# Kernel optimization log

Measured on AMD Instinct MI355X. Metric: run time of the kernel, lower is better.

## Reference

```python
import jax, jax.numpy as jnp
import numpy as np

NEG_SLOPE = 0.2  # GATConv default negative_slope


def gat_conv(x, row, col, W, b, a_src, a_dst, N):
    # GATConv, heads=1, flow='target_to_source': i=row (central), j=col (neighbor)
    h = x @ W                                                   # [N, C]
    e = jax.nn.leaky_relu((h @ a_src)[col] + (h @ a_dst)[row], NEG_SLOPE)  # [E]
    m = jax.ops.segment_max(e, row, num_segments=N)             # segment softmax over row
    w = jnp.exp(e - m[row])
    denom = jax.ops.segment_sum(w, row, num_segments=N)
    alpha = w / (denom[row] + 1e-16)
    out = jax.ops.segment_sum(alpha[:, None] * h[col], row, num_segments=N)
    return out + b


def lstm_scan(xs_t, Wih, Whh, bih, bhh):
    # xs_t: [L, N, C] -> hidden states [L, N, H]; PyTorch gate order i,f,g,o
    H = Whh.shape[1]
    Nn = xs_t.shape[1]
    bias = bih + bhh
    def step(carry, xt):
        h, c = carry
        g = xt @ Wih.T + h @ Whh.T + bias
        i, f, gg, o = jnp.split(g, 4, axis=-1)
        c = jax.nn.sigmoid(f) * c + jax.nn.sigmoid(i) * jnp.tanh(gg)
        h = jax.nn.sigmoid(o) * jnp.tanh(c)
        return (h, c), h
    init = (jnp.zeros((Nn, H), xs_t.dtype), jnp.zeros((Nn, H), xs_t.dtype))
    _, hs = jax.lax.scan(step, init, xs_t)
    return hs


def jk_lstm(xst, Wih_f, Whh_f, bih_f, bhh_f, Wih_b, Whh_b, bih_b, bhh_b, att_W, att_b):
    # xst: [L, N, C]; bidirectional LSTM over layer dim, attention-weighted sum
    hf = lstm_scan(xst, Wih_f, Whh_f, bih_f, bhh_f)
    hb = lstm_scan(xst[::-1], Wih_b, Whh_b, bih_b, bhh_b)[::-1]
    h = jnp.concatenate([hf, hb], axis=-1)                      # [L, N, 2H]
    score = jnp.einsum('lnh,h->ln', h, att_W) + att_b           # [L, N]
    alpha = jax.nn.softmax(score, axis=0)                       # softmax over layers
    return jnp.einsum('lnc,ln->nc', xst, alpha)                 # [N, C]


def setup_inputs() -> dict:
    key = jax.random.key(0)
    ks = list(jax.random.split(key, 32))
    N, E, C = 50000, 800000, 128
    L = 3
    H = (L * C) // 2  # 192; PyG JumpingKnowledge lstm hidden size
    s = 0.05
    d = {}
    d['x'] = jax.random.normal(ks[0], (N, 3), jnp.float32)
    d['edge_index'] = jax.random.randint(ks[1], (2, E), 0, N, jnp.int64)
    d['gat_W0'] = jax.random.normal(ks[2], (3, C)) * 0.3
    d['gat_b0'] = jnp.zeros((C,))
    d['gat_as0'] = jax.random.normal(ks[3], (C,)) * s
    d['gat_ad0'] = jax.random.normal(ks[4], (C,)) * s
    d['gat_W'] = jax.random.normal(ks[5], (L - 1, C, C)) * s
    d['gat_b'] = jnp.zeros((L - 1, C))
    d['gat_as'] = jax.random.normal(ks[6], (L - 1, C)) * s
    d['gat_ad'] = jax.random.normal(ks[7], (L - 1, C)) * s
    d['lstm_Wih_f'] = jax.random.normal(ks[8], (4 * H, C)) * s
    d['lstm_Whh_f'] = jax.random.normal(ks[9], (4 * H, H)) * s
    d['lstm_bih_f'] = jnp.zeros((4 * H,))
    d['lstm_bhh_f'] = jnp.zeros((4 * H,))
    d['lstm_Wih_b'] = jax.random.normal(ks[10], (4 * H, C)) * s
    d['lstm_Whh_b'] = jax.random.normal(ks[11], (4 * H, H)) * s
    d['lstm_bih_b'] = jnp.zeros((4 * H,))
    d['lstm_bhh_b'] = jnp.zeros((4 * H,))
    d['att_W'] = jax.random.normal(ks[12], (2 * H,)) * s
    d['att_b'] = jnp.zeros((1,))
    d['nW1'] = jax.random.normal(ks[13], (C, C)) * s
    d['nb1'] = jnp.zeros((C,))
    d['nW2'] = jax.random.normal(ks[14], (C, 2)) * s
    d['nb2'] = jnp.zeros((2,))
    d['eW1'] = jax.random.normal(ks[15], (2 * C, C)) * s
    d['eb1'] = jnp.zeros((C,))
    d['eW2'] = jax.random.normal(ks[16], (C, 2)) * s
    d['eb2'] = jnp.zeros((2,))
    return d


def reference(x, edge_index, gat_W0, gat_b0, gat_as0, gat_ad0, gat_W, gat_b, gat_as, gat_ad,
              lstm_Wih_f, lstm_Whh_f, lstm_bih_f, lstm_bhh_f,
              lstm_Wih_b, lstm_Whh_b, lstm_bih_b, lstm_bhh_b,
              att_W, att_b, nW1, nb1, nW2, nb2, eW1, eb1, eW2, eb2):
    N = x.shape[0]
    row, col = edge_index[0], edge_index[1]
    xs = []
    h = jax.nn.relu(gat_conv(x, row, col, gat_W0, gat_b0, gat_as0, gat_ad0, N))
    xs.append(h)
    for l in range(gat_W.shape[0]):  # fixed small layer count
        h = jax.nn.relu(gat_conv(h, row, col, gat_W[l], gat_b[l], gat_as[l], gat_ad[l], N))
        xs.append(h)
    xst = jnp.stack(xs, axis=0)  # [L, N, C]
    h = jk_lstm(xst, lstm_Wih_f, lstm_Whh_f, lstm_bih_f, lstm_bhh_f,
                lstm_Wih_b, lstm_Whh_b, lstm_bih_b, lstm_bhh_b, att_W, att_b)
    # node classifier (dropout is identity in eval)
    node_out = jax.nn.softmax(jax.nn.relu(h @ nW1 + nb1) @ nW2 + nb2, axis=1)
    # edge representation gather + concat, then edge classifier
    edge_rep = jnp.concatenate([h[row], h[col]], axis=1)  # [E, 2C]
    edge_out = jax.nn.softmax(jax.nn.relu(edge_rep @ eW1 + eb1) @ eW2 + eb2, axis=1)
    return node_out, edge_out
```

## Files before the change

kernel.cpp:

```cpp
#include <hip/hip_runtime.h>
#include <cstdint>
#include <cstddef>


#define NIN 28
#define MAXJOBS 20

struct InPtrs { const void* p[NIN]; int n[NIN]; };

struct ConvJobs {
    const void* src[MAXJOBS];
    float* dst[MAXJOBS];
    int n[MAXJOBS];
    int ai[MAXJOBS];
    int blk0[MAXJOBS + 1];
    int njobs;
};

typedef short s16x4 __attribute__((ext_vector_type(4)));
typedef short s16x8 __attribute__((ext_vector_type(8)));
typedef float f32x4 __attribute__((ext_vector_type(4)));
typedef unsigned short u16x8 __attribute__((ext_vector_type(8)));

__device__ __forceinline__ float bf2f(unsigned short v) {
    unsigned int u = ((unsigned int)v) << 16;
    return __uint_as_float(u);
}

__device__ __forceinline__ unsigned short f2bf(float x) {
    unsigned int u = __float_as_uint(x);
    unsigned int r = u + 0x7fffu + ((u >> 16) & 1u);
    return (unsigned short)(r >> 16);
}

__device__ __forceinline__ float rdx(const void* p, size_t i, int isf32) {
    return isf32 ? ((const float*)p)[i] : bf2f(((const unsigned short*)p)[i]);
}

__device__ __forceinline__ float frcp(float x) {
    return __builtin_amdgcn_rcpf(x);
}

__device__ __forceinline__ float sigm(float x) {
    return frcp(1.f + __expf(-x));
}

__device__ __forceinline__ float fast_tanh(float x) {
    return 1.f - 2.f * frcp(__expf(2.f * x) + 1.f);
}

__global__ void k_sniff(InPtrs in, int* flags) {
    int ai = blockIdx.x;
    if (ai >= NIN) return;
    __shared__ int cnt;
    if (threadIdx.x == 0) cnt = 0;
    __syncthreads();
    if (ai == 1) {
        const int* w = (const int*)in.p[1];
        int nw = in.n[1] < 512 ? in.n[1] : 512;
        int local = 0;
        for (int i = threadIdx.x; i < nw; i += blockDim.x)
            if ((i & 1) && w[i] != 0) local++;
        atomicAdd(&cnt, local);
        __syncthreads();
        if (threadIdx.x == 0) flags[1] = (cnt < 4) ? 1 : 0;
        return;
    }
    const unsigned short* u = (const unsigned short*)in.p[ai];
    int ns = in.n[ai] < 256 ? in.n[ai] : 256;
    int local = 0;
    for (int i = threadIdx.x; i < ns; i += blockDim.x) {
        if (i & 1) continue;
        unsigned short v = u[i];
        int e = (v >> 7) & 0xff;
        if ((v & 0x7fff) != 0 && (e < 100 || e > 154)) local++;
    }
    atomicAdd(&cnt, local);
    __syncthreads();
    if (threadIdx.x == 0) flags[ai] = (cnt * 4 >= ns) ? 1 : 0;
}

__global__ void k_convall(ConvJobs J, const int* __restrict__ flags) {
    int b = blockIdx.x;
    int j = 0;
    while (j + 1 < J.njobs && b >= J.blk0[j + 1]) ++j;
    int i = (b - J.blk0[j]) * 256 + threadIdx.x;
    if (i >= J.n[j]) return;
    J.dst[j][i] = rdx(J.src[j], i, flags[J.ai[j]]);
}

__global__ void k_conve(const void* src, int* row, int* col, int* cnt,
                        int E, const int* flags) {
    int i = blockIdx.x * blockDim.x + threadIdx.x;
    if (i >= E) return;
    int r, c;
    if (flags[1]) {
        const long long* s = (const long long*)src;
        r = (int)s[i];
        c = (int)s[(size_t)E + i];
    } else {
        const int* s = (const int*)src;
        r = s[i];
        c = s[(size_t)E + i];
    }
    row[i] = r;
    col[i] = c;
    atomicAdd(&cnt[r], 1);
}

__global__ void k_scan1(const int* __restrict__ deg, int* __restrict__ indptr,
                        int* __restrict__ bsums, int N) {
    __shared__ int buf[1024];
    const int t = threadIdx.x;
    const int base = blockIdx.x * 1024;
    int v = (base + t < N) ? deg[base + t] : 0;
    buf[t] = v;
    __syncthreads();
    for (int ofs = 1; ofs < 1024; ofs <<= 1) {
        int add = (t >= ofs) ? buf[t - ofs] : 0;
        __syncthreads();
        buf[t] += add;
        __syncthreads();
    }
    if (base + t < N) indptr[base + t] = buf[t] - v;
    if (t == 1023) bsums[blockIdx.x] = buf[1023];
}

__global__ void k_scan2(int* bsums, int nb) {
    if (threadIdx.x == 0 && blockIdx.x == 0) {
        int acc = 0;
        for (int j = 0; j < nb; ++j) { int v = bsums[j]; bsums[j] = acc; acc += v; }
        bsums[nb] = acc;
    }
}

__global__ void k_scan3(const int* __restrict__ bsums, int* __restrict__ indptr,
                        int* __restrict__ cnt, int N, int nb) {
    int i = blockIdx.x * blockDim.x + threadIdx.x;
    if (i < N) {
        indptr[i] += bsums[i >> 10];
        cnt[i] = 0;
    }
    if (i == 0) indptr[N] = bsums[nb];
}

__global__ void k_fill(const int* __restrict__ row, const int* __restrict__ col,
                       const int* __restrict__ indptr, int* __restrict__ cur,
                       int* __restrict__ colS, int* __restrict__ eidx, int E) {
    int i = blockIdx.x * blockDim.x + threadIdx.x;
    if (i >= E) return;
    int r = row[i];
    int p = indptr[r] + atomicAdd(&cur[r], 1);
    colS[p] = col[i];
    eidx[p] = i;
}

__global__ __launch_bounds__(256) void k_lin0(
    const float* __restrict__ x, const float* __restrict__ W0,
    const float* __restrict__ asrc, const float* __restrict__ adst,
    unsigned short* __restrict__ hlin, float* __restrict__ hs, float* __restrict__ hd,
    int N) {
    const int wid = threadIdx.x >> 6, lane = threadIdx.x & 63;
    const int n = blockIdx.x * 4 + wid;
    if (n >= N) return;
    float x0 = x[(size_t)n * 3], x1 = x[(size_t)n * 3 + 1], x2 = x[(size_t)n * 3 + 2];
    const int c0 = lane, c1 = lane + 64;
    float h0 = x0 * W0[c0] + x1 * W0[128 + c0] + x2 * W0[256 + c0];
    float h1 = x0 * W0[c1] + x1 * W0[128 + c1] + x2 * W0[256 + c1];
    hlin[(size_t)n * 128 + c0] = f2bf(h0);
    hlin[(size_t)n * 128 + c1] = f2bf(h1);
    float sp = h0 * asrc[c0] + h1 * asrc[c1];
    float dp = h0 * adst[c0] + h1 * adst[c1];
    for (int o = 32; o; o >>= 1) { sp += __shfl_down(sp, o); dp += __shfl_down(dp, o); }
    if (lane == 0) { hs[n] = sp; hd[n] = dp; }
}

__global__ void k_wpackg(const float* __restrict__ Wcanon,
                         unsigned short* __restrict__ Wg) {
    int idx = blockIdx.x * blockDim.x + threadIdx.x;
    if (idx >= 2 * 4 * 8 * 512) return;
    int layer = idx / 16384;
    int r  = idx % 16384;
    int kb = r / 4096;
    int r2 = r % 4096;
    int f  = r2 / 512;
    int q  = r2 % 512;
    int lane = q >> 3, j = q & 7;
    int k   = kb * 32 + ((j >> 2) * 16) + ((lane >> 4) * 4) + (j & 3);
    int col = f * 16 + (lane & 15);
    Wg[idx] = f2bf(Wcanon[(size_t)layer * 16384 + (size_t)k * 128 + col]);
}

__global__ __launch_bounds__(512) void k_linm(
    const unsigned short* __restrict__ xin,
    const unsigned short* __restrict__ Wg,
    const float* __restrict__ asrc, const float* __restrict__ adst,
    unsigned short* __restrict__ hlin, float* __restrict__ hs, float* __restrict__ hd,
    int N) {
    __shared__ unsigned short AS[64][136];
    __shared__ float hsS[64], hdS[64];
    const int t = threadIdx.x;
    const int f = t >> 6, lane = t & 63;
    const int n0 = blockIdx.x * 64;
    const int ccol = lane & 15;
    const int klane = lane >> 4;
    const int lrow = klane * 4;
    const int akl = klane * 4;
    const int m = f * 16 + ccol;

    const float asv = asrc[m], adv = adst[m];

    for (int i = t; i < 1024; i += 512) {
        int r = i >> 4, kq = (i & 15) * 8;
        u16x8 v = (u16x8)(0);
        if (n0 + r < N) v = *(const u16x8*)(xin + (size_t)(n0 + r) * 128 + kq);
        *(u16x8*)&AS[r][kq] = v;
    }
    if (t < 64) { hsS[t] = 0.f; hdS[t] = 0.f; }
    __syncthreads();

    f32x4 acc[4];
    #pragma unroll
    for (int rf = 0; rf < 4; ++rf) acc[rf] = (f32x4)(0.f);
    #pragma unroll
    for (int kb = 0; kb < 4; ++kb) {
        s16x8 b = *(const s16x8*)(Wg + ((size_t)kb * 8 + f) * 512 + lane * 8);
        const int k0 = kb * 32 + akl;
        #pragma unroll
        for (int rf = 0; rf < 4; ++rf) {
            s16x4 alo = *(const s16x4*)&AS[rf * 16 + ccol][k0];
            s16x4 ahi = *(const s16x4*)&AS[rf * 16 + ccol][k0 + 16];
            s16x8 av = __builtin_shufflevector(alo, ahi, 0, 1, 2, 3, 4, 5, 6, 7);
            acc[rf] = __builtin_amdgcn_mfma_f32_16x16x32_bf16(av, b, acc[rf], 0, 0, 0);
        }
    }
    __syncthreads();

    float sp[16], dp[16];
    #pragma unroll
    for (int rf = 0; rf < 4; ++rf) {
        #pragma unroll
        for (int reg = 0; reg < 4; ++reg) {
            float h = acc[rf][reg];
            int ci = rf * 4 + reg;
            AS[rf * 16 + lrow + reg][m] = f2bf(h);
            sp[ci] = h * asv;
            dp[ci] = h * adv;
        }
    }
    #pragma unroll
    for (int o = 1; o < 16; o <<= 1) {
        #pragma unroll
        for (int i = 0; i < 16; ++i) { sp[i] += __shfl_xor(sp[i], o); dp[i] += __shfl_xor(dp[i], o); }
    }
    if (ccol == 0) {
        #pragma unroll
        for (int i = 0; i < 16; ++i) {
            int row = (i >> 2) * 16 + lrow + (i & 3);
            atomicAdd(&hsS[row], sp[i]);
            atomicAdd(&hdS[row], dp[i]);
        }
    }
    __syncthreads();

    for (int i = t; i < 1024; i += 512) {
        int r = i >> 4, kq = (i & 15) * 8;
        if (n0 + r < N)
            *(u16x8*)(hlin + (size_t)(n0 + r) * 128 + kq) = *(const u16x8*)&AS[r][kq];
    }
    if (t < 64 && n0 + t < N) { hs[n0 + t] = hsS[t]; hd[n0 + t] = hdS[t]; }
}

__global__ __launch_bounds__(256) void k_aggr(
    const unsigned short* __restrict__ hlin, const float* __restrict__ hs,
    const float* __restrict__ hd,
    const int* __restrict__ indptr, const int* __restrict__ colS,
    const float* __restrict__ b, unsigned short* __restrict__ xout, int N) {
    const int wid = threadIdx.x >> 6, lane = threadIdx.x & 63;
    const int n = blockIdx.x * 4 + wid;
    if (n >= N) return;
    const int s = indptr[n], epos = indptr[n + 1];
    const float hdv = hd[n];
    const int c0 = lane, c1 = lane + 64;
    float m = -1e30f, d = 0.f, a0 = 0.f, a1 = 0.f;
    int idx = s;
    for (; idx + 8 <= epos; idx += 8) {
        int cl[8];
        #pragma unroll
        for (int j = 0; j < 8; ++j) cl[j] = colS[idx + j];
        float e[8];
        #pragma unroll
        for (int j = 0; j < 8; ++j) {
            float ev = hs[cl[j]] + hdv;
            e[j] = (ev > 0.f) ? ev : 0.2f * ev;
        }
        float v0[8], v1[8];
        #pragma unroll
        for (int j = 0; j < 8; ++j) {
            const unsigned short* hp = hlin + (size_t)cl[j] * 128;
            v0[j] = bf2f(hp[c0]);
            v1[j] = bf2f(hp[c1]);
        }
        float m8 = e[0];
        #pragma unroll
        for (int j = 1; j < 8; ++j) m8 = fmaxf(m8, e[j]);
        if (m8 > m) {
            float sc = __expf(m - m8);
            a0 *= sc; a1 *= sc; d *= sc; m = m8;
        }
        #pragma unroll
        for (int j = 0; j < 8; ++j) {
            float w = __expf(e[j] - m);
            a0 += w * v0[j];
            a1 += w * v1[j];
            d  += w;
        }
    }
    for (; idx < epos; ++idx) {
        int col = colS[idx];
        float e = hs[col] + hdv;
        e = (e > 0.f) ? e : 0.2f * e;
        const unsigned short* hr = hlin + (size_t)col * 128;
        float v0 = bf2f(hr[c0]), v1 = bf2f(hr[c1]);
        if (e > m) {
            float sc = __expf(m - e);
            a0 = a0 * sc + v0;
            a1 = a1 * sc + v1;
            d  = d * sc + 1.f;
            m  = e;
        } else {
            float w = __expf(e - m);
            a0 += w * v0;
            a1 += w * v1;
            d  += w;
        }
    }
    float inv = frcp(d + 1e-16f);
    float r0 = a0 * inv + b[c0];
    float r1 = a1 * inv + b[c1];
    xout[(size_t)n * 128 + c0] = f2bf(fmaxf(r0, 0.f));
    xout[(size_t)n * 128 + c1] = f2bf(fmaxf(r1, 0.f));
}

__global__ void k_wpack(const void* Wihf, const void* Whhf,
                        const void* Wihb, const void* Whhb,
                        const void* bihf, const void* bhhf,
                        const void* bihb, const void* bhhb,
                        const int* __restrict__ flags,
                        unsigned short* __restrict__ Bpack, float* __restrict__ bsum) {
    int idx = blockIdx.x * blockDim.x + threadIdx.x;
    const int TOT = 2 * 10 * 48 * 512;
    if (idx < TOT) {
        int dir = idx / (10 * 48 * 512);
        int r   = idx % (10 * 48 * 512);
        int kb  = r / (48 * 512);
        int r2  = r % (48 * 512);
        int f   = r2 / 512;
        int q   = r2 % 512;
        int lane = q >> 3, j = q & 7;
        int k   = kb * 32 + ((j >> 2) * 16) + ((lane >> 4) * 4) + (j & 3);
        int col = f * 16 + (lane & 15);
        float v;
        if (k < 128)
            v = dir ? rdx(Wihb, (size_t)col * 128 + k, flags[14])
                    : rdx(Wihf, (size_t)col * 128 + k, flags[10]);
        else
            v = dir ? rdx(Whhb, (size_t)col * 192 + (k - 128), flags[15])
                    : rdx(Whhf, (size_t)col * 192 + (k - 128), flags[11]);
        Bpack[idx] = f2bf(v);
    }
    if (idx < 2 * 768) {
        int d = idx / 768, j = idx % 768;
        bsum[idx] = d ? rdx(bihb, j, flags[16]) + rdx(bhhb, j, flags[17])
                      : rdx(bihf, j, flags[12]) + rdx(bhhf, j, flags[13]);
    }
}

__global__ __launch_bounds__(768, 3) void k_lstm_mfma(
    const unsigned short* __restrict__ xsb,
    const unsigned short* __restrict__ Bpack,
    const float* __restrict__ bsum,
    const float* __restrict__ attW,
    float* __restrict__ scoreP,
    int N) {
    __shared__ unsigned short AS[64][332];
    __shared__ float scoreS[64];
    const int t = threadIdx.x;
    const int bf = t >> 6, lane = t & 63;
    const int dir = blockIdx.y;
    const int n0 = blockIdx.x * 64;
    const int ccol = lane & 15;
    const int klane = lane >> 4;
    const int lrow = klane * 4;
    const int akl = klane * 4;
    const int m = bf * 16 + ccol;

    const float bI = bsum[dir * 768 + m];
    const float bF = bsum[dir * 768 + 192 + m];
    const float bG = bsum[dir * 768 + 384 + m];
    const float bO = bsum[dir * 768 + 576 + m];
    const float awt = attW[dir * 192 + m];
    float cst[16];
    #pragma unroll
    for (int i = 0; i < 16; ++i) cst[i] = 0.f;

    const unsigned short* Bd = Bpack + (size_t)dir * 10 * 48 * 512;

    for (int s = 0; s < 3; ++s) {
        const int l = dir ? (2 - s) : s;
        {
            const unsigned short* xsrc = xsb + ((size_t)l * N + n0) * 128;
            for (int i = t; i < 1024; i += 768) {
                int r = i >> 4, kq = (i & 15) * 8;
                u16x8 v = (u16x8)(0);
                if (n0 + r < N) v = *(const u16x8*)(xsrc + (size_t)r * 128 + kq);
                *(u16x8*)&AS[r][kq] = v;
            }
        }
        if (t < 64) scoreS[t] = 0.f;
        __syncthreads();

        const int KB = s ? 10 : 4;
        f32x4 acc[4][4];
        #pragma unroll
        for (int rf = 0; rf < 4; ++rf)
            #pragma unroll
            for (int g = 0; g < 4; ++g) acc[rf][g] = (f32x4)(0.f);
        s16x8 bA[4], bB[4];
        {
            const unsigned short* bb = Bd + (size_t)bf * 512 + lane * 8;
            #pragma unroll
            for (int g = 0; g < 4; ++g) bA[g] = *(const s16x8*)(bb + (size_t)g * 6144);
        }
        for (int kb = 0; kb < KB; kb += 2) {
            {
                const unsigned short* bb = Bd + ((size_t)(kb + 1) * 48 + bf) * 512 + lane * 8;
                #pragma unroll
                for (int g = 0; g < 4; ++g) bB[g] = *(const s16x8*)(bb + (size_t)g * 6144);
            }
            {
                const int k0 = kb * 32 + akl;
                s16x8 av[4];
                #pragma unroll
                for (int rf = 0; rf < 4; ++rf) {
                    s16x4 alo = *(const s16x4*)&AS[rf * 16 + ccol][k0];
                    s16x4 ahi = *(const s16x4*)&AS[rf * 16 + ccol][k0 + 16];
                    av[rf] = __builtin_shufflevector(alo, ahi, 0, 1, 2, 3, 4, 5, 6, 7);
                }
                #pragma unroll
                for (int rf = 0; rf < 4; ++rf)
                    #pragma unroll
                    for (int g = 0; g < 4; ++g)
                        acc[rf][g] = __builtin_amdgcn_mfma_f32_16x16x32_bf16(
                            av[rf], bA[g], acc[rf][g], 0, 0, 0);
            }
            if (kb + 2 < KB) {
                const unsigned short* bb = Bd + ((size_t)(kb + 2) * 48 + bf) * 512 + lane * 8;
                #pragma unroll
                for (int g = 0; g < 4; ++g) bA[g] = *(const s16x8*)(bb + (size_t)g * 6144);
            }
            {
                const int k0 = (kb + 1) * 32 + akl;
                s16x8 av[4];
                #pragma unroll
                for (int rf = 0; rf < 4; ++rf) {
                    s16x4 alo = *(const s16x4*)&AS[rf * 16 + ccol][k0];
                    s16x4 ahi = *(const s16x4*)&AS[rf * 16 + ccol][k0 + 16];
                    av[rf] = __builtin_shufflevector(alo, ahi, 0, 1, 2, 3, 4, 5, 6, 7);
                }
                #pragma unroll
                for (int rf = 0; rf < 4; ++rf)
                    #pragma unroll
                    for (int g = 0; g < 4; ++g)
                        acc[rf][g] = __builtin_amdgcn_mfma_f32_16x16x32_bf16(
                            av[rf], bB[g], acc[rf][g], 0, 0, 0);
            }
        }
        __syncthreads();

        float sp[16];
        #pragma unroll
        for (int rf = 0; rf < 4; ++rf) {
            #pragma unroll
            for (int reg = 0; reg < 4; ++reg) {
                float gI = acc[rf][0][reg] + bI;
                float gF = acc[rf][1][reg] + bF;
                float gG = acc[rf][2][reg] + bG;
                float gO = acc[rf][3][reg] + bO;
                float ig = sigm(gI);
                float fg = sigm(gF);
                float gt = fast_tanh(gG);
                float og = sigm(gO);
                int ci = rf * 4 + reg;
                float cn = fg * cst[ci] + ig * gt;
                cst[ci] = cn;
                float hh = og * fast_tanh(cn);
                AS[rf * 16 + lrow + reg][128 + m] = f2bf(hh);
                sp[ci] = hh * awt;
            }
        }
        #pragma unroll
        for (int o = 1; o < 16; o <<= 1) {
            #pragma unroll
            for (int i = 0; i < 16; ++i) sp[i] += __shfl_xor(sp[i], o);
        }
        if (ccol == 0) {
            #pragma unroll
            for (int i = 0; i < 16; ++i)
                atomicAdd(&scoreS[(i >> 2) * 16 + lrow + (i & 3)], sp[i]);
        }
        __syncthreads();
        if (t < 64 && n0 + t < N)
            scoreP[(size_t)(dir * 3 + l) * N + n0 + t] = scoreS[t];
    }
}

__global__ __launch_bounds__(256) void k_tail(
    const unsigned short* __restrict__ xsb, const float* __restrict__ scoreP,
    const float* __restrict__ nW1, const float* __restrict__ nb1,
    const float* __restrict__ nW2, const float* __restrict__ nb2,
    const float* __restrict__ eW1, const float* __restrict__ eb1,
    unsigned short* __restrict__ P, unsigned short* __restrict__ Q,
    float* __restrict__ out, int N) {
    __shared__ float xl[16][128];
    __shared__ float al[16][4];
    const int t = threadIdx.x;
    const int wid = t >> 6, lane = t & 63;
    const int nb = blockIdx.x * 16;
    if (t < 16) {
        int n = nb + t;
        float e0 = 0.f, e1 = 0.f, e2 = 0.f;
        if (n < N) {
            float s0 = scoreP[n]                 + scoreP[(size_t)3 * N + n];
            float s1 = scoreP[(size_t)N + n]     + scoreP[(size_t)4 * N + n];
            float s2 = scoreP[(size_t)2 * N + n] + scoreP[(size_t)5 * N + n];
            float mm = fmaxf(s0, fmaxf(s1, s2));
            e0 = __expf(s0 - mm); e1 = __expf(s1 - mm); e2 = __expf(s2 - mm);
            float inv = frcp(e0 + e1 + e2);
            e0 *= inv; e1 *= inv; e2 *= inv;
        }
        al[t][0] = e0; al[t][1] = e1; al[t][2] = e2;
    }
    __syncthreads();
    const size_t L1o = (size_t)N * 128, L2o = 2 * L1o;
    for (int i = t; i < 2048; i += 256) {
        int r = i >> 7, k = i & 127;
        int n = nb + r;
        float v = 0.f;
        if (n < N) {
            size_t p = (size_t)n * 128 + k;
            v = al[r][0] * bf2f(xsb[p]) + al[r][1] * bf2f(xsb[L1o + p])
              + al[r][2] * bf2f(xsb[L2o + p]);
        }
        xl[r][k] = v;
    }
    __syncthreads();
    const int c0 = lane, c1 = lane + 64;
    const int r0 = wid * 4;
    {
        float h0[4], h1[4];
        #pragma unroll
        for (int j = 0; j < 4; ++j) { h0[j] = 0.f; h1[j] = 0.f; }
        #pragma unroll 2
        for (int k = 0; k < 128; ++k) {
            float w0 = nW1[k * 128 + c0], w1 = nW1[k * 128 + c1];
            #pragma unroll
            for (int j = 0; j < 4; ++j) {
                float xv = xl[r0 + j][k];
                h0[j] += xv * w0;
                h1[j] += xv * w1;
            }
        }
        float p0[4], p1[4];
        #pragma unroll
        for (int j = 0; j < 4; ++j) {
            float a = fmaxf(h0[j] + nb1[c0], 0.f);
            float bq = fmaxf(h1[j] + nb1[c1], 0.f);
            p0[j] = a * nW2[c0 * 2 + 0] + bq * nW2[c1 * 2 + 0];
            p1[j] = a * nW2[c0 * 2 + 1] + bq * nW2[c1 * 2 + 1];
        }
        #pragma unroll
        for (int o = 32; o; o >>= 1) {
            #pragma unroll
            for (int j = 0; j < 4; ++j) {
                p0[j] += __shfl_down(p0[j], o);
                p1[j] += __shfl_down(p1[j], o);
            }
        }
        if (lane == 0) {
            #pragma unroll
            for (int j = 0; j < 4; ++j) {
                int n = nb + r0 + j;
                if (n < N) {
                    float l0 = p0[j] + nb2[0], l1 = p1[j] + nb2[1];
                    float mm = fmaxf(l0, l1);
                    float e0 = __expf(l0 - mm), e1 = __expf(l1 - mm);
                    float inv = frcp(e0 + e1);
                    out[2 * (size_t)n]     = e0 * inv;
                    out[2 * (size_t)n + 1] = e1 * inv;
                }
            }
        }
    }
    {
        float pp0[4], pp1[4], qq0[4], qq1[4];
        #pragma unroll
        for (int j = 0; j < 4; ++j) { pp0[j] = 0.f; pp1[j] = 0.f; qq0[j] = 0.f; qq1[j] = 0.f; }
        for (int k = 0; k < 128; ++k) {
            float wp0 = eW1[k * 128 + c0], wp1 = eW1[k * 128 + c1];
            float wq0 = eW1[(128 + k) * 128 + c0], wq1 = eW1[(128 + k) * 128 + c1];
            #pragma unroll
            for (int j = 0; j < 4; ++j) {
                float xv = xl[r0 + j][k];
                pp0[j] += xv * wp0; pp1[j] += xv * wp1;
                qq0[j] += xv * wq0; qq1[j] += xv * wq1;
            }
        }
        #pragma unroll
        for (int j = 0; j < 4; ++j) {
            int n = nb + r0 + j;
            if (n < N) {
                P[(size_t)n * 128 + c0] = f2bf(pp0[j] + eb1[c0]);
                P[(size_t)n * 128 + c1] = f2bf(pp1[j] + eb1[c1]);
                Q[(size_t)n * 128 + c0] = f2bf(qq0[j]);
                Q[(size_t)n * 128 + c1] = f2bf(qq1[j]);
            }
        }
    }
}

__global__ __launch_bounds__(256) void k_edge3(
    const unsigned short* __restrict__ P, const unsigned short* __restrict__ Q,
    const int* __restrict__ indptr, const int* __restrict__ colS,
    const int* __restrict__ eidx,
    const float* __restrict__ W2, const float* __restrict__ b2,
    float* __restrict__ out, int N) {
    const int wid = threadIdx.x >> 6, lane = threadIdx.x & 63;
    const int n = blockIdx.x * 4 + wid;
    if (n >= N) return;
    const int sl = lane & 15, g = lane >> 4;
    const int s = indptr[n], e = indptr[n + 1];
    float pf[8];
    {
        u16x8 pv = *(const u16x8*)(P + (size_t)n * 128 + sl * 8);
        #pragma unroll
        for (int j = 0; j < 8; ++j) pf[j] = bf2f(pv[j]);
    }
    const float* W2f = W2;
    const float b20 = b2[0], b21 = b2[1];
    for (int p = s + g; p < e; p += 8) {
        int p1 = p + 4;
        bool v1 = p1 < e;
        int col0 = colS[p],  eo0 = eidx[p];
        int col1 = v1 ? colS[p1] : col0;
        int eo1  = v1 ? eidx[p1] : 0;
        u16x8 qv0 = *(const u16x8*)(Q + (size_t)col0 * 128 + sl * 8);
        u16x8 qv1 = *(const u16x8*)(Q + (size_t)col1 * 128 + sl * 8);
        float l00 = 0.f, l01 = 0.f, l10 = 0.f, l11 = 0.f;
        #pragma unroll
        for (int j = 0; j < 8; ++j) {
            int ch = sl * 8 + j;
            float wA = W2f[ch * 2], wB = W2f[ch * 2 + 1];
            float h0 = fmaxf(pf[j] + bf2f(qv0[j]), 0.f);
            float h1 = fmaxf(pf[j] + bf2f(qv1[j]), 0.f);
            l00 += h0 * wA; l01 += h0 * wB;
            l10 += h1 * wA; l11 += h1 * wB;
        }
        #pragma unroll
        for (int o = 1; o < 16; o <<= 1) {
            l00 += __shfl_xor(l00, o); l01 += __shfl_xor(l01, o);
            l10 += __shfl_xor(l10, o); l11 += __shfl_xor(l11, o);
        }
        if (sl == 0) {
            {
                float a = l00 + b20, b = l01 + b21;
                float mm = fmaxf(a, b);
                float e0 = __expf(a - mm), e1 = __expf(b - mm);
                float inv = frcp(e0 + e1);
                out[2 * (size_t)N + 2 * (size_t)eo0]     = e0 * inv;
                out[2 * (size_t)N + 2 * (size_t)eo0 + 1] = e1 * inv;
            }
            if (v1) {
                float a = l10 + b20, b = l11 + b21;
                float mm = fmaxf(a, b);
                float e0 = __expf(a - mm), e1 = __expf(b - mm);
                float inv = frcp(e0 + e1);
                out[2 * (size_t)N + 2 * (size_t)eo1]     = e0 * inv;
                out[2 * (size_t)N + 2 * (size_t)eo1 + 1] = e1 * inv;
            }
        }
    }
}

extern "C" void kernel_launch(void* const* d_in, const int* in_sizes, int n_in,
                              void* d_out, int out_size, void* d_ws, size_t ws_size,
                              hipStream_t stream) {
    if (n_in < NIN) return;
    const int N = in_sizes[0] / 3;
    const int E = in_sizes[1] / 2;

    char* ws = (char*)d_ws;
    size_t off = 0;
    auto alloc = [&](size_t bytes) -> char* {
        char* p = ws + off;
        off = (off + bytes + 255) & ~(size_t)255;
        return p;
    };
    int* flags = (int*)alloc(32 * sizeof(int));
    int* bsums = (int*)alloc(128 * sizeof(int));
    float* canon[NIN];
    for (int i = 0; i < NIN; ++i) canon[i] = nullptr;
    for (int i = 0; i < NIN; ++i) {
        if (i == 1 || (i >= 10 && i <= 17)) continue;
        canon[i] = (float*)alloc((size_t)in_sizes[i] * 4);
    }
    int* row32  = (int*)alloc((size_t)E * 4);
    int* col32  = (int*)alloc((size_t)E * 4);
    int* indptr = (int*)alloc((size_t)(N + 1) * 4);
    int* cnt    = (int*)alloc((size_t)N * 4);
    int* colS   = (int*)alloc((size_t)E * 4);
    int* eidx   = (int*)alloc((size_t)E * 4);
    float* hs   = (float*)alloc((size_t)N * 4);
    float* hd   = (float*)alloc((size_t)N * 4);
    float* hJK  = (float*)alloc((size_t)N * 128 * 4);
    unsigned short* hlin = (unsigned short*)hJK;
    unsigned short* xsb = (unsigned short*)alloc((size_t)3 * N * 128 * 2);
    unsigned short* Bpack = (unsigned short*)alloc((size_t)2 * 10 * 48 * 512 * 2);
    unsigned short* Wg = (unsigned short*)alloc((size_t)2 * 4 * 8 * 512 * 2);
    float* bsum = (float*)alloc((size_t)2 * 768 * 4);
    float* scoreP = (float*)alloc((size_t)6 * N * 4);
    if (off > ws_size) return;
    unsigned short* P = (unsigned short*)hJK;
    unsigned short* Q = (unsigned short*)hJK + (size_t)N * 128;

    InPtrs ip;
    for (int i = 0; i < NIN; ++i) { ip.p[i] = d_in[i]; ip.n[i] = in_sizes[i]; }

    k_sniff<<<NIN, 256, 0, stream>>>(ip, flags);

    {
        ConvJobs J;
        int nj = 0, blk = 0;
        for (int i = 0; i < NIN; ++i) {
            if (i == 1 || (i >= 10 && i <= 17)) continue;
            J.src[nj] = d_in[i];
            J.dst[nj] = canon[i];
            J.n[nj] = in_sizes[i];
            J.ai[nj] = i;
            J.blk0[nj] = blk;
            blk += (in_sizes[i] + 255) / 256;
            ++nj;
        }
        J.blk0[nj] = blk;
        J.njobs = nj;
        k_convall<<<blk, 256, 0, stream>>>(J, flags);
    }
    hipMemsetAsync(cnt, 0, (size_t)N * 4, stream);
    k_conve<<<(E + 255) / 256, 256, 0, stream>>>(d_in[1], row32, col32, cnt, E, flags);
    k_wpack<<<(2 * 10 * 48 * 512 + 255) / 256, 256, 0, stream>>>(
        d_in[10], d_in[11], d_in[14], d_in[15],
        d_in[12], d_in[13], d_in[16], d_in[17], flags, Bpack, bsum);
    k_wpackg<<<(2 * 4 * 8 * 512 + 255) / 256, 256, 0, stream>>>(canon[6], Wg);

    const int nb1k = (N + 1023) / 1024;
    k_scan1<<<nb1k, 1024, 0, stream>>>(cnt, indptr, bsums, N);
    k_scan2<<<1, 64, 0, stream>>>(bsums, nb1k);
    k_scan3<<<(N + 255) / 256, 256, 0, stream>>>(bsums, indptr, cnt, N, nb1k);
    k_fill<<<(E + 255) / 256, 256, 0, stream>>>(row32, col32, indptr, cnt, colS, eidx, E);

    k_lin0<<<(N + 3) / 4, 256, 0, stream>>>(canon[0], canon[2], canon[4], canon[5],
                                            hlin, hs, hd, N);
    k_aggr<<<(N + 3) / 4, 256, 0, stream>>>(hlin, hs, hd, indptr, colS, canon[3], xsb, N);
    for (int l = 1; l < 3; ++l) {
        const unsigned short* Wgl = Wg + (size_t)(l - 1) * 4 * 8 * 512;
        const float* bb = canon[7] + (size_t)(l - 1) * 128;
        const float* as = canon[8] + (size_t)(l - 1) * 128;
        const float* ad = canon[9] + (size_t)(l - 1) * 128;
        k_linm<<<(N + 63) / 64, 512, 0, stream>>>(xsb + (size_t)(l - 1) * N * 128, Wgl,
                                                  as, ad, hlin, hs, hd, N);
        k_aggr<<<(N + 3) / 4, 256, 0, stream>>>(hlin, hs, hd, indptr, colS, bb,
                                                xsb + (size_t)l * N * 128, N);
    }

    dim3 lgrid((N + 63) / 64, 2);
    k_lstm_mfma<<<lgrid, 768, 0, stream>>>(xsb, Bpack, bsum, canon[18], scoreP, N);

    float* out = (float*)d_out;
    k_tail<<<(N + 15) / 16, 256, 0, stream>>>(xsb, scoreP,
                                              canon[20], canon[21], canon[22], canon[23],
                                              canon[24], canon[25], P, Q, out, N);
    k_edge3<<<(N + 3) / 4, 256, 0, stream>>>(P, Q, indptr, colS, eidx,
                                             canon[26], canon[27], out, N);
}
```

Measured before the change: 671.7 us.

## Move tail node and edge-projection GEMMs onto bf16 MFMA with packed weights

Replaces the scalar-FMA k_tail kernel with k_tailm, which blends the three layer outputs into a bf16 LDS tile of 64 nodes and computes the node-classifier hidden layer and both edge projections (P and Q) with 16x16x32 bf16 MFMA instructions. A new packing kernel pre-arranges nW1 and both halves of eW1 into the MFMA fragment layout. Outputs are staged through LDS for vectorized coalesced stores, and the node logits are reduced with shuffles and LDS atomics. The aim is to remove the FP32 scalar-FMA cost of three 128x128 GEMMs per node. The trade-off is bf16 rounding of the blended activations and of the weights.

```diff
diff --git a/kernel.cpp b/kernel.cpp
--- a/kernel.cpp
+++ b/kernel.cpp
@@ -189,6 +189,25 @@
     int k   = kb * 32 + ((j >> 2) * 16) + ((lane >> 4) * 4) + (j & 3);
     int col = f * 16 + (lane & 15);
     Wg[idx] = f2bf(Wcanon[(size_t)layer * 16384 + (size_t)k * 128 + col]);
+}
+
+__global__ void k_wpackt(const float* __restrict__ nW1, const float* __restrict__ eW1,
+                         unsigned short* __restrict__ Wt) {
+    int idx = blockIdx.x * blockDim.x + threadIdx.x;
+    if (idx >= 4 * 24 * 512) return;
+    int kb = idx / (24 * 512);
+    int r  = idx % (24 * 512);
+    int fr = r / 512;
+    int q  = r % 512;
+    int lane = q >> 3, j = q & 7;
+    int k   = kb * 32 + ((j >> 2) * 16) + ((lane >> 4) * 4) + (j & 3);
+    int grp = fr >> 3;
+    int col = (fr & 7) * 16 + (lane & 15);
+    float v;
+    if (grp == 0)      v = nW1[(size_t)k * 128 + col];
+    else if (grp == 1) v = eW1[(size_t)k * 128 + col];
+    else               v = eW1[(size_t)(128 + k) * 128 + col];
+    Wt[idx] = f2bf(v);
 }
 
 __global__ __launch_bounds__(512) void k_linm(
@@ -515,20 +534,27 @@
     }
 }
 
-__global__ __launch_bounds__(256) void k_tail(
+__global__ __launch_bounds__(512) void k_tailm(
     const unsigned short* __restrict__ xsb, const float* __restrict__ scoreP,
-    const float* __restrict__ nW1, const float* __restrict__ nb1,
-    const float* __restrict__ nW2, const float* __restrict__ nb2,
-    const float* __restrict__ eW1, const float* __restrict__ eb1,
+    const unsigned short* __restrict__ Wt,
+    const float* __restrict__ nb1, const float* __restrict__ nW2,
+    const float* __restrict__ nb2, const float* __restrict__ eb1,
     unsigned short* __restrict__ P, unsigned short* __restrict__ Q,
     float* __restrict__ out, int N) {
-    __shared__ float xl[16][128];
-    __shared__ float al[16][4];
+    __shared__ unsigned short AS[64][136];
+    __shared__ float al[64][4];
+    __shared__ float lgt[64][2];
     const int t = threadIdx.x;
-    const int wid = t >> 6, lane = t & 63;
-    const int nb = blockIdx.x * 16;
-    if (t < 16) {
-        int n = nb + t;
+    const int f = t >> 6, lane = t & 63;
+    const int n0 = blockIdx.x * 64;
+    const int ccol = lane & 15;
+    const int klane = lane >> 4;
+    const int lrow = klane * 4;
+    const int akl = klane * 4;
+    const int m = f * 16 + ccol;
+
+    if (t < 64) {
+        int n = n0 + t;
         float e0 = 0.f, e1 = 0.f, e2 = 0.f;
         if (n < N) {
             float s0 = scoreP[n]                 + scoreP[(size_t)3 * N + n];
@@ -540,92 +566,110 @@
             e0 *= inv; e1 *= inv; e2 *= inv;
         }
         al[t][0] = e0; al[t][1] = e1; al[t][2] = e2;
-    }
-    __syncthreads();
+        lgt[t][0] = 0.f; lgt[t][1] = 0.f;
+    }
+    __syncthreads();
+
     const size_t L1o = (size_t)N * 128, L2o = 2 * L1o;
-    for (int i = t; i < 2048; i += 256) {
-        int r = i >> 7, k = i & 127;
-        int n = nb + r;
-        float v = 0.f;
-        if (n < N) {
-            size_t p = (size_t)n * 128 + k;
-            v = al[r][0] * bf2f(xsb[p]) + al[r][1] * bf2f(xsb[L1o + p])
-              + al[r][2] * bf2f(xsb[L2o + p]);
-        }
-        xl[r][k] = v;
-    }
-    __syncthreads();
-    const int c0 = lane, c1 = lane + 64;
-    const int r0 = wid * 4;
+    for (int i = t; i < 1024; i += 512) {
+        int r = i >> 4, kq = (i & 15) * 8;
+        u16x8 o8 = (u16x8)(0);
+        if (n0 + r < N) {
+            size_t base = (size_t)(n0 + r) * 128 + kq;
+            u16x8 a = *(const u16x8*)(xsb + base);
+            u16x8 b = *(const u16x8*)(xsb + L1o + base);
+            u16x8 c = *(const u16x8*)(xsb + L2o + base);
+            float w0 = al[r][0], w1 = al[r][1], w2 = al[r][2];
+            #pragma unroll
+            for (int j = 0; j < 8; ++j)
+                o8[j] = f2bf(w0 * bf2f(a[j]) + w1 * bf2f(b[j]) + w2 * bf2f(c[j]));
+        }
+        *(u16x8*)&AS[r][kq] = o8;
+    }
+    __syncthreads();
+
+    f32x4 accN[4], accP[4], accQ[4];
+    #pragma unroll
+    for (int rf = 0; rf < 4; ++rf) { accN[rf] = (f32x4)(0.f); accP[rf] = (f32x4)(0.f); accQ[rf] = (f32x4)(0.f); }
+    #pragma unroll
+    for (int kb = 0; kb < 4; ++kb) {
+        s16x8 bN = *(const s16x8*)(Wt + ((size_t)kb * 24 + f) * 512 + lane * 8);
+        s16x8 bP = *(const s16x8*)(Wt + ((size_t)kb * 24 + 8 + f) * 512 + lane * 8);
+        s16x8 bQ = *(const s16x8*)(Wt + ((size_t)kb * 24 + 16 + f) * 512 + lane * 8);
+        const int k0 = kb * 32 + akl;
+        #pragma unroll
+        for (int rf = 0; rf < 4; ++rf) {
+            s16x4 alo = *(const s16x4*)&AS[rf * 16 + ccol][k0];
+            s16x4 ahi = *(const s16x4*)&AS[rf * 16 + ccol][k0 + 16];
+            s16x8 av = __builtin_shufflevector(alo, ahi, 0, 1, 2, 3, 4, 5, 6, 7);
+            accN[rf] = __builtin_amdgcn_mfma_f32_16x16x32_bf16(av, bN, accN[rf], 0, 0, 0);
+            accP[rf] = __builtin_amdgcn_mfma_f32_16x16x32_bf16(av, bP, accP[rf], 0, 0, 0);
+            accQ[rf] = __builtin_amdgcn_mfma_f32_16x16x32_bf16(av, bQ, accQ[rf], 0, 0, 0);
+        }
+    }
+    __syncthreads();
+
     {
-        float h0[4], h1[4];
-        #pragma unroll
-        for (int j = 0; j < 4; ++j) { h0[j] = 0.f; h1[j] = 0.f; }
-        #pragma unroll 2
-        for (int k = 0; k < 128; ++k) {
-            float w0 = nW1[k * 128 + c0], w1 = nW1[k * 128 + c1];
-            #pragma unroll
-            for (int j = 0; j < 4; ++j) {
-                float xv = xl[r0 + j][k];
-                h0[j] += xv * w0;
-                h1[j] += xv * w1;
-            }
-        }
-        float p0[4], p1[4];
-        #pragma unroll
-        for (int j = 0; j < 4; ++j) {
-            float a = fmaxf(h0[j] + nb1[c0], 0.f);
-            float bq = fmaxf(h1[j] + nb1[c1], 0.f);
-            p0[j] = a * nW2[c0 * 2 + 0] + bq * nW2[c1 * 2 + 0];
-            p1[j] = a * nW2[c0 * 2 + 1] + bq * nW2[c1 * 2 + 1];
-        }
-        #pragma unroll
-        for (int o = 32; o; o >>= 1) {
-            #pragma unroll
-            for (int j = 0; j < 4; ++j) {
-                p0[j] += __shfl_down(p0[j], o);
-                p1[j] += __shfl_down(p1[j], o);
-            }
-        }
-        if (lane == 0) {
-            #pragma unroll
-            for (int j = 0; j < 4; ++j) {
-                int n = nb + r0 + j;
-                if (n < N) {
-                    float l0 = p0[j] + nb2[0], l1 = p1[j] + nb2[1];
-                    float mm = fmaxf(l0, l1);
-                    float e0 = __expf(l0 - mm), e1 = __expf(l1 - mm);
-                    float inv = frcp(e0 + e1);
-                    out[2 * (size_t)n]     = e0 * inv;
-                    out[2 * (size_t)n + 1] = e1 * inv;
-                }
+        const float nb1v = nb1[m];
+        const float w20 = nW2[2 * m], w21 = nW2[2 * m + 1];
+        float s0[16], s1[16];
+        #pragma unroll
+        for (int rf = 0; rf < 4; ++rf) {
+            #pragma unroll
+            for (int reg = 0; reg < 4; ++reg) {
+                float h = fmaxf(accN[rf][reg] + nb1v, 0.f);
+                int ci = rf * 4 + reg;
+                s0[ci] = h * w20;
+                s1[ci] = h * w21;
+            }
+        }
+        #pragma unroll
+        for (int o = 1; o < 16; o <<= 1) {
+            #pragma unroll
+            for (int i = 0; i < 16; ++i) { s0[i] += __shfl_xor(s0[i], o); s1[i] += __shfl_xor(s1[i], o); }
+        }
+        if (ccol == 0) {
+            #pragma unroll
+            for (int i = 0; i < 16; ++i) {
+                int row = (i >> 2) * 16 + lrow + (i & 3);
+                atomicAdd(&lgt[row][0], s0[i]);
+                atomicAdd(&lgt[row][1], s1[i]);
             }
         }
     }
     {
-        float pp0[4], pp1[4], qq0[4], qq1[4];
-        #pragma unroll
-        for (int j = 0; j < 4; ++j) { pp0[j] = 0.f; pp1[j] = 0.f; qq0[j] = 0.f; qq1[j] = 0.f; }
-        for (int k = 0; k < 128; ++k) {
-            float wp0 = eW1[k * 128 + c0], wp1 = eW1[k * 128 + c1];
-            float wq0 = eW1[(128 + k) * 128 + c0], wq1 = eW1[(128 + k) * 128 + c1];
-            #pragma unroll
-            for (int j = 0; j < 4; ++j) {
-                float xv = xl[r0 + j][k];
-                pp0[j] += xv * wp0; pp1[j] += xv * wp1;
-                qq0[j] += xv * wq0; qq1[j] += xv * wq1;
-            }
-        }
-        #pragma unroll
-        for (int j = 0; j < 4; ++j) {
-            int n = nb + r0 + j;
-            if (n < N) {
-                P[(size_t)n * 128 + c0] = f2bf(pp0[j] + eb1[c0]);
-                P[(size_t)n * 128 + c1] = f2bf(pp1[j] + eb1[c1]);
-                Q[(size_t)n * 128 + c0] = f2bf(qq0[j]);
-                Q[(size_t)n * 128 + c1] = f2bf(qq1[j]);
-            }
-        }
+        const float eb1v = eb1[m];
+        #pragma unroll
+        for (int rf = 0; rf < 4; ++rf)
+            #pragma unroll
+            for (int reg = 0; reg < 4; ++reg)
+                AS[rf * 16 + lrow + reg][m] = f2bf(accP[rf][reg] + eb1v);
+    }
+    __syncthreads();
+    if (t < 64 && n0 + t < N) {
+        float l0 = lgt[t][0] + nb2[0], l1 = lgt[t][1] + nb2[1];
+        float mm = fmaxf(l0, l1);
+        float e0 = __expf(l0 - mm), e1 = __expf(l1 - mm);
+        float inv = frcp(e0 + e1);
+        out[2 * (size_t)(n0 + t)]     = e0 * inv;
+        out[2 * (size_t)(n0 + t) + 1] = e1 * inv;
+    }
+    for (int i = t; i < 1024; i += 512) {
+        int r = i >> 4, kq = (i & 15) * 8;
+        if (n0 + r < N)
+            *(u16x8*)(P + (size_t)(n0 + r) * 128 + kq) = *(const u16x8*)&AS[r][kq];
+    }
+    __syncthreads();
+    #pragma unroll
+    for (int rf = 0; rf < 4; ++rf)
+        #pragma unroll
+        for (int reg = 0; reg < 4; ++reg)
+            AS[rf * 16 + lrow + reg][m] = f2bf(accQ[rf][reg]);
+    __syncthreads();
+    for (int i = t; i < 1024; i += 512) {
+        int r = i >> 4, kq = (i & 15) * 8;
+        if (n0 + r < N)
+            *(u16x8*)(Q + (size_t)(n0 + r) * 128 + kq) = *(const u16x8*)&AS[r][kq];
     }
 }
 
@@ -727,6 +771,7 @@
     unsigned short* xsb = (unsigned short*)alloc((size_t)3 * N * 128 * 2);
     unsigned short* Bpack = (unsigned short*)alloc((size_t)2 * 10 * 48 * 512 * 2);
     unsigned short* Wg = (unsigned short*)alloc((size_t)2 * 4 * 8 * 512 * 2);
+    unsigned short* Wt = (unsigned short*)alloc((size_t)4 * 24 * 512 * 2);
     float* bsum = (float*)alloc((size_t)2 * 768 * 4);
     float* scoreP = (float*)alloc((size_t)6 * N * 4);
     if (off > ws_size) return;
@@ -761,6 +806,7 @@
         d_in[10], d_in[11], d_in[14], d_in[15],
         d_in[12], d_in[13], d_in[16], d_in[17], flags, Bpack, bsum);
     k_wpackg<<<(2 * 4 * 8 * 512 + 255) / 256, 256, 0, stream>>>(canon[6], Wg);
+    k_wpackt<<<(4 * 24 * 512 + 255) / 256, 256, 0, stream>>>(canon[20], canon[24], Wt);
 
     const int nb1k = (N + 1023) / 1024;
     k_scan1<<<nb1k, 1024, 0, stream>>>(cnt, indptr, bsums, N);
@@ -786,9 +832,9 @@
     k_lstm_mfma<<<lgrid, 768, 0, stream>>>(xsb, Bpack, bsum, canon[18], scoreP, N);
 
     float* out = (float*)d_out;
-    k_tail<<<(N + 15) / 16, 256, 0, stream>>>(xsb, scoreP,
-                                              canon[20], canon[21], canon[22], canon[23],
-                                              canon[24], canon[25], P, Q, out, N);
+    k_tailm<<<(N + 63) / 64, 512, 0, stream>>>(xsb, scoreP, Wt,
+                                               canon[21], canon[22], canon[23], canon[25],
+                                               P, Q, out, N);
     k_edge3<<<(N + 3) / 4, 256, 0, stream>>>(P, Q, indptr, colS, eidx,
                                              canon[26], canon[27], out, N);
 }
```

Measured after the change: 594.9 us. 1.13x faster.
